# Optimization experiments

Measured on AMD Instinct MI355X. Metric: run time of the kernel, lower is better.

The kernel has to match this reference:

```python
import jax, jax.numpy as jnp
import numpy as np

DIM = 2048
N_HEADS = 16
HEAD_DIM = DIM // N_HEADS  # 128
KV_RANK = 512
MAX_SEQ = 2048
EPS = 1e-6


def _precompute_freqs(dim, end, theta=10000.0):
    freqs = 1.0 / theta ** (np.arange(0, dim, 2)[: dim // 2].astype(np.float32) / dim)
    t = np.arange(end, dtype=np.float32)
    ang = np.outer(t, freqs)  # [end, dim//2]
    return jnp.asarray(np.cos(ang)), jnp.asarray(np.sin(ang))


def setup_inputs() -> dict:
    key = jax.random.key(0)
    ks = jax.random.split(key, 6)
    s = 0.02
    x = jax.random.normal(ks[0], (1, 2048, DIM), dtype=jnp.float32)
    wq = jax.random.normal(ks[1], (N_HEADS * HEAD_DIM, DIM), dtype=jnp.float32) * s
    w_kv_down = jax.random.normal(ks[2], (KV_RANK, DIM), dtype=jnp.float32) * s
    w_kv_up = jax.random.normal(ks[3], (2 * N_HEADS * HEAD_DIM, KV_RANK), dtype=jnp.float32) * s
    wo = jax.random.normal(ks[4], (DIM, N_HEADS * HEAD_DIM), dtype=jnp.float32) * s
    q_norm_w = jnp.ones((HEAD_DIM,), dtype=jnp.float32)
    k_norm_w = jnp.ones((HEAD_DIM,), dtype=jnp.float32)
    freqs_cos, freqs_sin = _precompute_freqs(HEAD_DIM, MAX_SEQ)
    return {"x": x, "wq": wq, "w_kv_down": w_kv_down, "w_kv_up": w_kv_up,
            "wo": wo, "q_norm_w": q_norm_w, "k_norm_w": k_norm_w,
            "freqs_cos": freqs_cos, "freqs_sin": freqs_sin}


def _rmsnorm(x, w):
    var = jnp.mean(x * x, axis=-1, keepdims=True)
    return x * jax.lax.rsqrt(var + EPS) * w


def _rope(x, cos, sin):
    # x: [B,T,H,D] -> pairs [B,T,H,D/2,2]; cos/sin: [T,D/2] broadcast over heads
    xr = x.reshape(*x.shape[:-1], -1, 2)
    re, im = xr[..., 0], xr[..., 1]
    c = cos[None, :, None, :]
    s = sin[None, :, None, :]
    out = jnp.stack([re * c - im * s, re * s + im * c], axis=-1)
    return out.reshape(x.shape)


def reference(x, wq, w_kv_down, w_kv_up, wo, q_norm_w, k_norm_w, freqs_cos, freqs_sin):
    B, T, C = x.shape
    H, D = N_HEADS, HEAD_DIM
    xq = jnp.einsum('btc,ec->bte', x, wq).reshape(B, T, H, D)
    latent = jnp.einsum('btc,rc->btr', x, w_kv_down)            # [B,T,R]
    kv = jnp.einsum('btr,er->bte', latent, w_kv_up).reshape(B, T, 2, H, D)
    xk, xv = kv[:, :, 0], kv[:, :, 1]
    xq = _rmsnorm(xq, q_norm_w)
    xk = _rmsnorm(xk, k_norm_w)
    cos, sin = freqs_cos[:T], freqs_sin[:T]
    xq = _rope(xq, cos, sin)
    xk = _rope(xk, cos, sin)
    scale = 1.0 / jnp.sqrt(jnp.asarray(D, dtype=x.dtype))
    scores = jnp.einsum('bthd,bshd->bhts', xq, xk) * scale       # [B,H,T,T]
    causal = jnp.tril(jnp.ones((T, T), dtype=bool))
    scores = jnp.where(causal, scores, jnp.finfo(scores.dtype).min)
    attn = jax.nn.softmax(scores, axis=-1)
    out = jnp.einsum('bhts,bshd->bthd', attn, xv).reshape(B, T, C)
    return jnp.einsum('bte,ce->btc', out, wo)
```

## Files before the change

### kernel.cpp

```cpp
#include <hip/hip_runtime.h>

#define T_SEQ 2048
#define DIM   2048
#define NH    16
#define HD    128
#define KVR   512

typedef unsigned short ushort_t;
typedef __attribute__((ext_vector_type(8))) short   short8;
typedef __attribute__((ext_vector_type(8))) __bf16  bf16x8;
typedef __attribute__((ext_vector_type(4))) float   f32x4;
typedef __attribute__((ext_vector_type(4))) unsigned int u32x4;

union V8 { short8 s; bf16x8 b; u32x4 u; };

__device__ inline float b2f(ushort_t u) {
    union { unsigned u; float f; } x; x.u = ((unsigned)u) << 16; return x.f;
}
__device__ inline ushort_t f2b(float f) {
    union { float f; unsigned u; } x; x.f = f;
    unsigned r = x.u + 0x7FFFu + ((x.u >> 16) & 1u);
    return (ushort_t)(r >> 16);
}

__device__ __forceinline__ void gld16(char* lds, const ushort_t* g) {
    __builtin_amdgcn_global_load_lds(
        (const __attribute__((address_space(1))) unsigned int*)g,
        (__attribute__((address_space(3))) unsigned int*)lds,
        16, 0, 0);
}

__global__ __launch_bounds__(256) void cvtk(
    const float* __restrict__ a0, const float* __restrict__ a1,
    const float* __restrict__ a2, const float* __restrict__ a3,
    const float* __restrict__ a4,
    ushort_t* __restrict__ b0, ushort_t* __restrict__ b1,
    ushort_t* __restrict__ b2, ushort_t* __restrict__ b3,
    ushort_t* __restrict__ b4)
{
    const int N0 = 524288, N1 = 1048576, N2 = 1179648, N3 = 1441792, N4 = 1966080;
    for (int c = blockIdx.x * blockDim.x + threadIdx.x; c < N4; c += gridDim.x * blockDim.x) {
        const float* s; ushort_t* d; int off;
        if      (c < N0) { s = a0; d = b0; off = c; }
        else if (c < N1) { s = a1; d = b1; off = c - N0; }
        else if (c < N2) { s = a2; d = b2; off = c - N1; }
        else if (c < N3) { s = a3; d = b3; off = c - N2; }
        else             { s = a4; d = b4; off = c - N3; }
        f32x4 lo = *(const f32x4*)(s + (size_t)off * 8);
        f32x4 hi = *(const f32x4*)(s + (size_t)off * 8 + 4);
        V8 v;
        #pragma unroll
        for (int e = 0; e < 4; ++e) { v.b[e] = (__bf16)lo[e]; v.b[e + 4] = (__bf16)hi[e]; }
        *(u32x4*)(d + (size_t)off * 8) = v.u;
    }
}

template <bool OUT_F32>
__global__ __launch_bounds__(256) void gemm_nt(
    const ushort_t* __restrict__ A, const ushort_t* __restrict__ B,
    void* __restrict__ Cv, int M, int K,
    const ushort_t* __restrict__ B2, void* __restrict__ C2, int Nsplit, int N2)
{
    __shared__ __align__(16) char sA[2][16384];
    __shared__ __align__(16) char sB[2][16384];

    const int tid  = threadIdx.x;
    const int wave = tid >> 6;
    const int lane = tid & 63;
    const int l15  = lane & 15;
    const int l4   = lane >> 4;
    const int bm   = blockIdx.x * 128;
    const int bn   = blockIdx.y * 128;

    const ushort_t* Bp = B;
    void* Cp = Cv; int ldC = Nsplit; int bnl = bn;
    if (B2 != nullptr && bn >= Nsplit) { Bp = B2; Cp = C2; ldC = N2; bnl = bn - Nsplit; }

    const int wm = (wave >> 1) * 64;
    const int wn = (wave & 1) * 64;

    const int lp   = lane ^ ((lane >> 3) & 7);
    const int prow = lp >> 3;
    const int psub = lp & 7;
    const ushort_t* aSrc[4];
    const ushort_t* bSrc[4];
    #pragma unroll
    for (int i = 0; i < 4; ++i) {
        int r = wave * 32 + i * 8 + prow;
        aSrc[i] = A  + (size_t)(bm  + r) * K + psub * 8;
        bSrc[i] = Bp + (size_t)(bnl + r) * K + psub * 8;
    }
    const int ldsOff = wave * 4096;

    f32x4 acc[4][4] = {};
    const int nk = K >> 6;

    #pragma unroll
    for (int i = 0; i < 4; ++i) {
        gld16(&sA[0][ldsOff + i * 1024], aSrc[i]);
        gld16(&sB[0][ldsOff + i * 1024], bSrc[i]);
    }

    int cur = 0;
    for (int k = 0; k < nk; ++k) {
        __syncthreads();
        if (k + 1 < nk) {
            const int ko = (k + 1) * 64;
            #pragma unroll
            for (int i = 0; i < 4; ++i) {
                gld16(&sA[cur ^ 1][ldsOff + i * 1024], aSrc[i] + ko);
                gld16(&sB[cur ^ 1][ldsOff + i * 1024], bSrc[i] + ko);
            }
        }
        #pragma unroll
        for (int kk = 0; kk < 2; ++kk) {
            V8 a[4], b[4];
            #pragma unroll
            for (int i2 = 0; i2 < 4; ++i2) {
                int row = wm + i2 * 16 + l15;
                a[i2].u = *(const u32x4*)(sA[cur] + ((row * 128 + kk * 64 + l4 * 16) ^ ((row & 7) << 4)));
                int col = wn + i2 * 16 + l15;
                b[i2].u = *(const u32x4*)(sB[cur] + ((col * 128 + kk * 64 + l4 * 16) ^ ((col & 7) << 4)));
            }
            #pragma unroll
            for (int i2 = 0; i2 < 4; ++i2)
                #pragma unroll
                for (int j = 0; j < 4; ++j)
                    acc[i2][j] = __builtin_amdgcn_mfma_f32_16x16x32_bf16(a[i2].b, b[j].b, acc[i2][j], 0, 0, 0);
        }
        cur ^= 1;
    }

    #pragma unroll
    for (int i = 0; i < 4; ++i)
        #pragma unroll
        for (int j = 0; j < 4; ++j)
            #pragma unroll
            for (int r = 0; r < 4; ++r) {
                int rowg = bm + wm + i * 16 + l4 * 4 + r;
                int colg = bnl + wn + j * 16 + l15;
                if constexpr (OUT_F32)
                    ((float*)Cp)[(size_t)rowg * ldC + colg] = acc[i][j][r];
                else
                    ((ushort_t*)Cp)[(size_t)rowg * ldC + colg] = f2b(acc[i][j][r]);
            }
}

__global__ __launch_bounds__(256) void norm_rope2(
    ushort_t* __restrict__ Qb, ushort_t* __restrict__ KVb,
    const float* __restrict__ QW, const float* __restrict__ KW,
    const float* __restrict__ FC, const float* __restrict__ FS)
{
    const int b    = blockIdx.x;
    const bool isK = b >= 2048;
    const int t    = b & 2047;
    const int tid  = threadIdx.x;
    const int h    = tid >> 4;
    const int sub  = tid & 15;

    ushort_t* X        = isK ? KVb : Qb;
    const float* W     = isK ? KW : QW;
    const int stride   = isK ? 4096 : 2048;

    ushort_t* p = X + (size_t)t * stride + h * HD + sub * 8;
    V8 v; v.u = *(const u32x4*)p;
    float f[8];
    #pragma unroll
    for (int e = 0; e < 8; ++e) f[e] = b2f((ushort_t)v.s[e]);

    float ss = 0.f;
    #pragma unroll
    for (int e = 0; e < 8; ++e) ss += f[e] * f[e];
    ss += __shfl_xor(ss, 1);
    ss += __shfl_xor(ss, 2);
    ss += __shfl_xor(ss, 4);
    ss += __shfl_xor(ss, 8);
    float inv = rsqrtf(ss * (1.0f / 128.0f) + 1e-6f);

    float outv[8];
    #pragma unroll
    for (int k = 0; k < 4; ++k) {
        float c  = FC[(size_t)t * 64 + sub * 4 + k];
        float s  = FS[(size_t)t * 64 + sub * 4 + k];
        float w0 = W[sub * 8 + 2 * k];
        float w1 = W[sub * 8 + 2 * k + 1];
        float re = f[2 * k] * inv * w0;
        float im = f[2 * k + 1] * inv * w1;
        outv[2 * k]     = re * c - im * s;
        outv[2 * k + 1] = re * s + im * c;
    }
    V8 o;
    #pragma unroll
    for (int e = 0; e < 8; ++e) o.s[e] = (short)f2b(outv[e]);
    *(u32x4*)p = o.u;
}

#define STAGE_LOAD(kv0) do { \
  _Pragma("unroll") for (int rr = 0; rr < 4; ++rr) \
    kreg[rr] = *(const u32x4*)(KV + (size_t)((kv0) + krow[rr]) * (2 * DIM) + h * HD + kc8 * 8); \
  _Pragma("unroll") for (int rr = 0; rr < 2; ++rr) \
    _Pragma("unroll") for (int e = 0; e < 8; ++e) \
      vreg[rr][e] = *(const unsigned*)(KV + (size_t)((kv0) + vkvb[rr] * 8 + e) * (2 * DIM) + DIM + h * HD + vd); \
} while (0)

#define STAGE_WRITE(sKb, sVb) do { \
  _Pragma("unroll") for (int rr = 0; rr < 4; ++rr) \
    *(u32x4*)((sKb) + ((krow[rr] * 256 + kc8 * 16) ^ ((krow[rr] & 7) << 4))) = kreg[rr]; \
  _Pragma("unroll") for (int rr = 0; rr < 2; ++rr) { \
    V8 lo, hi; \
    _Pragma("unroll") for (int e = 0; e < 8; ++e) { \
      lo.s[e] = (short)(vreg[rr][e] & 0xFFFFu); hi.s[e] = (short)(vreg[rr][e] >> 16); } \
    *(u32x4*)((sVb) + ((vd * 128 + vkvb[rr] * 16) ^ ((vd & 7) << 4)))             = lo.u; \
    *(u32x4*)((sVb) + (((vd + 1) * 128 + vkvb[rr] * 16) ^ (((vd + 1) & 7) << 4))) = hi.u; \
  } \
} while (0)

__global__ __launch_bounds__(512) void attn_kernel(
    const ushort_t* __restrict__ Q,
    const ushort_t* __restrict__ KV,
    ushort_t* __restrict__ O)
{
    __shared__ __align__(16) char sAll[131072];

    const int id    = blockIdx.x;
    const int xcd   = id & 7;
    const int slot  = id >> 3;
    const int h     = xcd * 2 + (slot >> 4);
    const int pairb = slot & 15;

    const int tid   = threadIdx.x;
    const int gid   = tid >> 8;
    const int wtid  = tid & 255;
    const int wave4 = wtid >> 6;
    const int lane  = tid & 63;
    const int Qq    = lane & 15;
    const int G     = lane >> 4;

    char* gbase = sAll + gid * 65536;

    const int krow[4] = { (0*256 + wtid) >> 4, (1*256 + wtid) >> 4,
                          (2*256 + wtid) >> 4, (3*256 + wtid) >> 4 };
    const int kc8 = wtid & 15;
    const int vd  = lane * 2;
    const int vkvb[2] = { wave4, 4 + wave4 };

    const float scale = 0.08838834764831845f;

    u32x4 kreg[4];
    unsigned vreg[2][8];

    #pragma unroll
    for (int phase = 0; phase < 2; ++phase) {
        const int jt  = phase ? (31 - pairb) : pairb;
        const int q0w = jt * 64 + wave4 * 16;

        V8 qf[4];
        #pragma unroll
        for (int kk = 0; kk < 4; ++kk)
            qf[kk].u = *(const u32x4*)(Q + (size_t)(q0w + Qq) * DIM + h * HD + kk * 32 + G * 8);

        f32x4 o[8] = {};
        float mrow = -1e30f, lrow = 0.f;

        const int n_g = (jt >= gid) ? ((jt - gid) >> 1) + 1 : 0;
        const int nA  = (jt >> 1) + 1;

        if (n_g > 0) {
            STAGE_LOAD(gid * 64);
            STAGE_WRITE(gbase, gbase + 32768);
        }

        int cur = 0;
        for (int s = 0; s < nA; ++s) {
            __syncthreads();

            const bool pf = (s + 1 < n_g);
            if (pf) STAGE_LOAD((2 * (s + 1) + gid) * 64);

            if (s < n_g) {
                const int tcur = 2 * s + gid;
                const int kv0  = tcur * 64;
                char* sKb = gbase + cur * 16384;
                char* sVb = gbase + 32768 + cur * 16384;

                f32x4 sacc[4] = {};
                #pragma unroll
                for (int kk = 0; kk < 4; ++kk) {
                    #pragma unroll
                    for (int cb = 0; cb < 4; ++cb) {
                        int row = cb * 16 + Qq;
                        V8 kf;
                        kf.u = *(const u32x4*)(sKb + ((row * 256 + kk * 64 + G * 16) ^ ((row & 7) << 4)));
                        sacc[cb] = __builtin_amdgcn_mfma_f32_16x16x32_bf16(kf.b, qf[kk].b, sacc[cb], 0, 0, 0);
                    }
                }

                float p[4][4];
                float tmax = -3e38f;
                const int qg = q0w + Qq;
                #pragma unroll
                for (int cb = 0; cb < 4; ++cb)
                    #pragma unroll
                    for (int r = 0; r < 4; ++r) {
                        float s2 = sacc[cb][r] * scale;
                        if (tcur == jt) {
                            int kvg = kv0 + cb * 16 + G * 4 + r;
                            if (kvg > qg) s2 = -1e30f;
                        }
                        p[cb][r] = s2;
                        tmax = fmaxf(tmax, s2);
                    }
                tmax = fmaxf(tmax, __shfl_xor(tmax, 16));
                tmax = fmaxf(tmax, __shfl_xor(tmax, 32));
                float mnew = fmaxf(mrow, tmax);
                float corr = __expf(mrow - mnew);
                mrow = mnew;
                float rs = 0.f;
                #pragma unroll
                for (int cb = 0; cb < 4; ++cb)
                    #pragma unroll
                    for (int r = 0; r < 4; ++r) {
                        float e = __expf(p[cb][r] - mnew);
                        p[cb][r] = e;
                        rs += e;
                    }
                rs += __shfl_xor(rs, 16);
                rs += __shfl_xor(rs, 32);
                lrow = lrow * corr + rs;

                unsigned pk[4][2];
                #pragma unroll
                for (int cb = 0; cb < 4; ++cb) {
                    pk[cb][0] = (unsigned)f2b(p[cb][0]) | ((unsigned)f2b(p[cb][1]) << 16);
                    pk[cb][1] = (unsigned)f2b(p[cb][2]) | ((unsigned)f2b(p[cb][3]) << 16);
                }

                float cf[4];
                #pragma unroll
                for (int r = 0; r < 4; ++r)
                    cf[r] = __shfl(corr, G * 4 + r);
                #pragma unroll
                for (int nb = 0; nb < 8; ++nb)
                    #pragma unroll
                    for (int r = 0; r < 4; ++r)
                        o[nb][r] *= cf[r];

                const int sLo = ((G & 1) * 2) * 16 + Qq;
                const int sHi = sLo + 16;
                const bool hiC = (G >> 1);
                #pragma unroll
                for (int kk2 = 0; kk2 < 2; ++kk2) {
                    const int c0 = kk2 * 2, c1 = c0 + 1;
                    unsigned w0a = __shfl(pk[c0][0], sLo), w0b = __shfl(pk[c1][0], sLo);
                    unsigned w1a = __shfl(pk[c0][1], sLo), w1b = __shfl(pk[c1][1], sLo);
                    unsigned w2a = __shfl(pk[c0][0], sHi), w2b = __shfl(pk[c1][0], sHi);
                    unsigned w3a = __shfl(pk[c0][1], sHi), w3b = __shfl(pk[c1][1], sHi);
                    V8 pa;
                    pa.u[0] = hiC ? w0b : w0a;
                    pa.u[1] = hiC ? w1b : w1a;
                    pa.u[2] = hiC ? w2b : w2a;
                    pa.u[3] = hiC ? w3b : w3a;
                    #pragma unroll
                    for (int nb = 0; nb < 8; ++nb) {
                        int d = nb * 16 + Qq;
                        V8 vf;
                        vf.u = *(const u32x4*)(sVb + ((d * 128 + kk2 * 64 + G * 16) ^ ((d & 7) << 4)));
                        o[nb] = __builtin_amdgcn_mfma_f32_16x16x32_bf16(pa.b, vf.b, o[nb], 0, 0, 0);
                    }
                }
            }

            if (pf) STAGE_WRITE(gbase + (cur ^ 1) * 16384, gbase + 32768 + (cur ^ 1) * 16384);
            cur ^= 1;
        }

        __syncthreads();
        float* mrg = (float*)sAll;
        float* mlb = (float*)(sAll + 33792);
        if (gid == 1) {
            #pragma unroll
            for (int nb = 0; nb < 8; ++nb)
                #pragma unroll
                for (int r = 0; r < 4; ++r) {
                    int qloc = wave4 * 16 + G * 4 + r;
                    mrg[qloc * 132 + nb * 16 + Qq] = o[nb][r];
                }
            if (G == 0) {
                int qloc = wave4 * 16 + Qq;
                mlb[qloc]      = mrow;
                mlb[64 + qloc] = lrow;
            }
        }
        __syncthreads();
        if (gid == 0) {
            int qloc0 = wave4 * 16 + Qq;
            float mB = mlb[qloc0], lB = mlb[64 + qloc0];
            float m  = fmaxf(mrow, mB);
            float cA = __expf(mrow - m), cB = __expf(mB - m);
            float linv = 1.f / (lrow * cA + lB * cB);
            float cAr[4], cBr[4], lir[4];
            #pragma unroll
            for (int r = 0; r < 4; ++r) {
                cAr[r] = __shfl(cA, G * 4 + r);
                cBr[r] = __shfl(cB, G * 4 + r);
                lir[r] = __shfl(linv, G * 4 + r);
            }
            #pragma unroll
            for (int nb = 0; nb < 8; ++nb)
                #pragma unroll
                for (int r = 0; r < 4; ++r) {
                    int qloc = wave4 * 16 + G * 4 + r;
                    float ob  = mrg[qloc * 132 + nb * 16 + Qq];
                    float val = (o[nb][r] * cAr[r] + ob * cBr[r]) * lir[r];
                    int qgr = jt * 64 + qloc;
                    O[(size_t)qgr * DIM + h * HD + nb * 16 + Qq] = f2b(val);
                }
        }
        __syncthreads();
    }
}

extern "C" void kernel_launch(void* const* d_in, const int* in_sizes, int n_in,
                              void* d_out, int out_size, void* d_ws, size_t ws_size,
                              hipStream_t stream)
{
    const float* x    = (const float*)d_in[0];
    const float* wq   = (const float*)d_in[1];
    const float* wkvd = (const float*)d_in[2];
    const float* wkvu = (const float*)d_in[3];
    const float* wo   = (const float*)d_in[4];
    const float* qnw  = (const float*)d_in[5];
    const float* knw  = (const float*)d_in[6];
    const float* fc   = (const float*)d_in[7];
    const float* fs   = (const float*)d_in[8];
    float* out = (float*)d_out;

    char* ws = (char*)d_ws;
    const size_t MB = 1024 * 1024;
    ushort_t* xb    = (ushort_t*)(ws);
    ushort_t* att   = (ushort_t*)(ws);
    ushort_t* Qb    = (ushort_t*)(ws + 8  * MB);
    ushort_t* wqb   = (ushort_t*)(ws + 16 * MB);
    ushort_t* wkvdb = (ushort_t*)(ws + 24 * MB);
    ushort_t* kvb   = (ushort_t*)(ws + 16 * MB);
    ushort_t* lat   = (ushort_t*)(ws + 32 * MB);
    ushort_t* wkvub = (ushort_t*)(ws + 34 * MB);
    ushort_t* wob   = (ushort_t*)(ws + 38 * MB);

    cvtk<<<dim3(2048), dim3(256), 0, stream>>>(x, wq, wkvd, wkvu, wo,
                                               xb, wqb, wkvdb, wkvub, wob);
    gemm_nt<false><<<dim3(16, 20), dim3(256), 0, stream>>>(xb, wqb, Qb, 2048, 2048,
                                                           wkvdb, lat, 2048, 512);
    gemm_nt<false><<<dim3(16, 32), dim3(256), 0, stream>>>(lat, wkvub, kvb, 2048, 512,
                                                           nullptr, nullptr, 4096, 0);
    norm_rope2<<<dim3(4096), dim3(256), 0, stream>>>(Qb, kvb, qnw, knw, fc, fs);
    attn_kernel<<<dim3(256), dim3(512), 0, stream>>>(Qb, kvb, att);
    gemm_nt<true><<<dim3(16, 16), dim3(256), 0, stream>>>(att, wob, out, 2048, 2048,
                                                          nullptr, nullptr, 2048, 0);
}
```

Before: 171.2 us.

## Split attention KV loop across four wave groups with single-buffered LDS and priority hints

The attention block grows from 512 to 1024 threads, so four groups of four waves each take every fourth KV tile instead of two groups taking alternating tiles. To fit in shared memory, each group's LDS staging is cut from double-buffered to single-buffered with an extra barrier per iteration, and the final merge combines four partial softmax states. The change also adds s_setprio around the MFMA loops and a waves-per-EU hint on the GEMM kernel. It aims for more parallelism per tile and better latency hiding, at the cost of losing LDS double-buffer overlap, more barriers and higher register pressure at 1024 threads.

```diff
diff --git a/kernel.cpp b/kernel.cpp
--- a/kernel.cpp
+++ b/kernel.cpp
@@ -56,7 +56,7 @@
 }
 
 template <bool OUT_F32>
-__global__ __launch_bounds__(256) void gemm_nt(
+__global__ __launch_bounds__(256, 2) void gemm_nt(
     const ushort_t* __restrict__ A, const ushort_t* __restrict__ B,
     void* __restrict__ Cv, int M, int K,
     const ushort_t* __restrict__ B2, void* __restrict__ C2, int Nsplit, int N2)
@@ -215,7 +215,7 @@
   } \
 } while (0)
 
-__global__ __launch_bounds__(512) void attn_kernel(
+__global__ __launch_bounds__(1024, 4) void attn_kernel(
     const ushort_t* __restrict__ Q,
     const ushort_t* __restrict__ KV,
     ushort_t* __restrict__ O)
@@ -236,7 +236,7 @@
     const int Qq    = lane & 15;
     const int G     = lane >> 4;
 
-    char* gbase = sAll + gid * 65536;
+    char* gbase = sAll + gid * 32768;
 
     const int krow[4] = { (0*256 + wtid) >> 4, (1*256 + wtid) >> 4,
                           (2*256 + wtid) >> 4, (3*256 + wtid) >> 4 };
@@ -249,6 +249,14 @@
     u32x4 kreg[4];
     unsigned vreg[2][8];
 
+    float* aO[3]; float* aM[3]; float* aL[3];
+    #pragma unroll
+    for (int g = 0; g < 3; ++g) {
+        aO[g] = (float*)(sAll + g * 34816);
+        aM[g] = (float*)(sAll + g * 34816 + 33792);
+        aL[g] = (float*)(sAll + g * 34816 + 34048);
+    }
+
     #pragma unroll
     for (int phase = 0; phase < 2; ++phase) {
         const int jt  = phase ? (31 - pairb) : pairb;
@@ -262,28 +270,25 @@
         f32x4 o[8] = {};
         float mrow = -1e30f, lrow = 0.f;
 
-        const int n_g = (jt >= gid) ? ((jt - gid) >> 1) + 1 : 0;
-        const int nA  = (jt >> 1) + 1;
-
-        if (n_g > 0) {
-            STAGE_LOAD(gid * 64);
-            STAGE_WRITE(gbase, gbase + 32768);
-        }
-
-        int cur = 0;
-        for (int s = 0; s < nA; ++s) {
+        const int n_g  = (jt >= gid) ? ((jt - gid) >> 2) + 1 : 0;
+        const int nMax = (jt >> 2) + 1;
+
+        if (n_g > 0) STAGE_LOAD(gid * 64);
+
+        for (int s = 0; s < nMax; ++s) {
             __syncthreads();
-
-            const bool pf = (s + 1 < n_g);
-            if (pf) STAGE_LOAD((2 * (s + 1) + gid) * 64);
+            if (s < n_g) STAGE_WRITE(gbase, gbase + 16384);
+            __syncthreads();
+            if (s + 1 < n_g) STAGE_LOAD((4 * (s + 1) + gid) * 64);
 
             if (s < n_g) {
-                const int tcur = 2 * s + gid;
+                const int tcur = 4 * s + gid;
                 const int kv0  = tcur * 64;
-                char* sKb = gbase + cur * 16384;
-                char* sVb = gbase + 32768 + cur * 16384;
+                char* sKb = gbase;
+                char* sVb = gbase + 16384;
 
                 f32x4 sacc[4] = {};
+                __builtin_amdgcn_s_setprio(1);
                 #pragma unroll
                 for (int kk = 0; kk < 4; ++kk) {
                     #pragma unroll
@@ -294,6 +299,7 @@
                         sacc[cb] = __builtin_amdgcn_mfma_f32_16x16x32_bf16(kf.b, qf[kk].b, sacc[cb], 0, 0, 0);
                     }
                 }
+                __builtin_amdgcn_s_setprio(0);
 
                 float p[4][4];
                 float tmax = -3e38f;
@@ -360,6 +366,7 @@
                     pa.u[1] = hiC ? w1b : w1a;
                     pa.u[2] = hiC ? w2b : w2a;
                     pa.u[3] = hiC ? w3b : w3a;
+                    __builtin_amdgcn_s_setprio(1);
                     #pragma unroll
                     for (int nb = 0; nb < 8; ++nb) {
                         int d = nb * 16 + Qq;
@@ -367,54 +374,50 @@
                         vf.u = *(const u32x4*)(sVb + ((d * 128 + kk2 * 64 + G * 16) ^ ((d & 7) << 4)));
                         o[nb] = __builtin_amdgcn_mfma_f32_16x16x32_bf16(pa.b, vf.b, o[nb], 0, 0, 0);
                     }
+                    __builtin_amdgcn_s_setprio(0);
                 }
             }
-
-            if (pf) STAGE_WRITE(gbase + (cur ^ 1) * 16384, gbase + 32768 + (cur ^ 1) * 16384);
-            cur ^= 1;
         }
 
         __syncthreads();
-        float* mrg = (float*)sAll;
-        float* mlb = (float*)(sAll + 33792);
-        if (gid == 1) {
+        if (gid >= 1) {
+            float* mO = aO[gid - 1];
             #pragma unroll
             for (int nb = 0; nb < 8; ++nb)
                 #pragma unroll
                 for (int r = 0; r < 4; ++r) {
                     int qloc = wave4 * 16 + G * 4 + r;
-                    mrg[qloc * 132 + nb * 16 + Qq] = o[nb][r];
+                    mO[qloc * 132 + nb * 16 + Qq] = o[nb][r];
                 }
             if (G == 0) {
                 int qloc = wave4 * 16 + Qq;
-                mlb[qloc]      = mrow;
-                mlb[64 + qloc] = lrow;
+                aM[gid - 1][qloc] = mrow;
+                aL[gid - 1][qloc] = lrow;
             }
         }
         __syncthreads();
         if (gid == 0) {
-            int qloc0 = wave4 * 16 + Qq;
-            float mB = mlb[qloc0], lB = mlb[64 + qloc0];
-            float m  = fmaxf(mrow, mB);
-            float cA = __expf(mrow - m), cB = __expf(mB - m);
-            float linv = 1.f / (lrow * cA + lB * cB);
-            float cAr[4], cBr[4], lir[4];
             #pragma unroll
             for (int r = 0; r < 4; ++r) {
-                cAr[r] = __shfl(cA, G * 4 + r);
-                cBr[r] = __shfl(cB, G * 4 + r);
-                lir[r] = __shfl(linv, G * 4 + r);
-            }
-            #pragma unroll
-            for (int nb = 0; nb < 8; ++nb)
-                #pragma unroll
-                for (int r = 0; r < 4; ++r) {
-                    int qloc = wave4 * 16 + G * 4 + r;
-                    float ob  = mrg[qloc * 132 + nb * 16 + Qq];
-                    float val = (o[nb][r] * cAr[r] + ob * cBr[r]) * lir[r];
+                int qloc = wave4 * 16 + G * 4 + r;
+                float m0 = __shfl(mrow, G * 4 + r);
+                float l0 = __shfl(lrow, G * 4 + r);
+                float m1 = aM[0][qloc], m2 = aM[1][qloc], m3 = aM[2][qloc];
+                float l1 = aL[0][qloc], l2 = aL[1][qloc], l3 = aL[2][qloc];
+                float mt = fmaxf(fmaxf(m0, m1), fmaxf(m2, m3));
+                float c0 = __expf(m0 - mt), c1 = __expf(m1 - mt);
+                float c2 = __expf(m2 - mt), c3 = __expf(m3 - mt);
+                float li = 1.f / (l0 * c0 + l1 * c1 + l2 * c2 + l3 * c3);
+                #pragma unroll
+                for (int nb = 0; nb < 8; ++nb) {
+                    float v = o[nb][r] * c0
+                            + aO[0][qloc * 132 + nb * 16 + Qq] * c1
+                            + aO[1][qloc * 132 + nb * 16 + Qq] * c2
+                            + aO[2][qloc * 132 + nb * 16 + Qq] * c3;
                     int qgr = jt * 64 + qloc;
-                    O[(size_t)qgr * DIM + h * HD + nb * 16 + Qq] = f2b(val);
+                    O[(size_t)qgr * DIM + h * HD + nb * 16 + Qq] = f2b(v * li);
                 }
+            }
         }
         __syncthreads();
     }
@@ -454,7 +457,7 @@
     gemm_nt<false><<<dim3(16, 32), dim3(256), 0, stream>>>(lat, wkvub, kvb, 2048, 512,
                                                            nullptr, nullptr, 4096, 0);
     norm_rope2<<<dim3(4096), dim3(256), 0, stream>>>(Qb, kvb, qnw, knw, fc, fs);
-    attn_kernel<<<dim3(256), dim3(512), 0, stream>>>(Qb, kvb, att);
+    attn_kernel<<<dim3(256), dim3(1024), 0, stream>>>(Qb, kvb, att);
     gemm_nt<true><<<dim3(16, 16), dim3(256), 0, stream>>>(att, wob, out, 2048, 2048,
                                                           nullptr, nullptr, 2048, 0);
 }
```

After: 274.4 us. +60.3%, slower.
